# Performance work log

Measured on AMD Instinct MI355X. Metric: run time of the kernel, lower is better.

Reference implementation:

```python
import jax, jax.numpy as jnp
import numpy as np

GROUPS = 16
GROUP_SIZE = 16
K = 3
KK = K * K
BN_EPS = 1e-5


def setup_inputs() -> dict:
    key = jax.random.key(0)
    ks = jax.random.split(key, 6)
    B, C, H, W = 16, 256, 56, 56
    mid = C // 4  # rd_ratio = 4
    x = jax.random.normal(ks[0], (B, C, H, W), dtype=jnp.float32)
    w1 = jax.random.normal(ks[1], (mid, C), dtype=jnp.float32) * (1.0 / np.sqrt(C))
    bn_gamma = jnp.ones((mid,), dtype=jnp.float32)
    bn_beta = jnp.zeros((mid,), dtype=jnp.float32)
    bn_mean = jax.random.normal(ks[2], (mid,), dtype=jnp.float32) * 0.1
    bn_var = jax.random.uniform(ks[3], (mid,), dtype=jnp.float32, minval=0.5, maxval=1.5)
    w2 = jax.random.normal(ks[4], (KK * GROUPS, mid), dtype=jnp.float32) * (1.0 / np.sqrt(mid))
    b2 = jax.random.normal(ks[5], (KK * GROUPS,), dtype=jnp.float32) * 0.01
    return {"x": x, "w1": w1, "bn_gamma": bn_gamma, "bn_beta": bn_beta,
            "bn_mean": bn_mean, "bn_var": bn_var, "w2": w2, "b2": b2}


def reference(x, w1, bn_gamma, bn_beta, bn_mean, bn_var, w2, b2):
    B, C, H, W = x.shape
    # conv1: 1x1 conv + BatchNorm (eval) + ReLU
    t = jnp.einsum('bchw,oc->bohw', x, w1)
    scale = bn_gamma / jnp.sqrt(bn_var + BN_EPS)
    t = t * scale[None, :, None, None] + (bn_beta - bn_mean * scale)[None, :, None, None]
    t = jax.nn.relu(t)
    # conv2: 1x1 conv producing per-pixel kernels (B, KK*groups, H, W)
    weight = jnp.einsum('bchw,oc->bohw', t, w2) + b2[None, :, None, None]
    weight = weight.reshape(B, GROUPS, 1, KK, H, W)
    # unfold: extract 3x3 patches (pad=1, stride=1), kernel positions row-major
    xp = jnp.pad(x, ((0, 0), (0, 0), (1, 1), (1, 1)))
    patches = jnp.stack(
        [xp[:, :, i:i + H, j:j + W] for i in range(K) for j in range(K)],
        axis=2)  # (B, C, KK, H, W), matches torch unfold's (c*KK + kk) layout
    patches = patches.reshape(B, GROUPS, GROUP_SIZE, KK, H, W)
    out = (weight * patches).sum(axis=3).reshape(B, C, H, W)
    return out
```

## Files before the change

kernel.cpp:

```cpp
#include <hip/hip_runtime.h>


#define Cn    256
#define MID   64
#define Hn    56
#define Wn    56
#define HW    3136
#define Bn    16
#define NPIX  (Bn * HW)
#define CHW   (Cn * HW)
#define NKK   9
#define NG    16
#define GSZ   16
#define PXT   64
#define BN_EPS 1e-5f

__global__ __launch_bounds__(256) void prep_kernel(
    const float* __restrict__ w1,
    const float* __restrict__ gamma,
    const float* __restrict__ beta,
    const float* __restrict__ mean,
    const float* __restrict__ var,
    float* __restrict__ w1f,
    float* __restrict__ bias1) {
  int idx = blockIdx.x * 256 + threadIdx.x;
  if (idx < MID * Cn) {
    int c = idx >> 6;
    int o = idx & 63;
    float scale = gamma[o] / sqrtf(var[o] + BN_EPS);
    w1f[idx] = w1[o * Cn + c] * scale;
  } else if (idx < MID * Cn + MID) {
    int o = idx - MID * Cn;
    float scale = gamma[o] / sqrtf(var[o] + BN_EPS);
    bias1[o] = beta[o] - mean[o] * scale;
  }
}

__global__ __launch_bounds__(256) void conv1_kernel(
    const float* __restrict__ x,
    const float* __restrict__ w1f,
    const float* __restrict__ bias1,
    float* __restrict__ t) {
  __shared__ float lx[2][16][PXT];

  int tid = threadIdx.x;
  int px  = tid & 63;
  int ocv = tid >> 6;
  int oc  = __builtin_amdgcn_readfirstlane(ocv);

  int px0 = blockIdx.x * PXT;
  int b   = px0 / HW;
  int hw0 = px0 - b * HW;
  const float* xb = x + (size_t)b * CHW + hw0;

  float r[4];
#pragma unroll
  for (int j = 0; j < 4; ++j) {
    int c = j * 4 + ocv;
    r[j] = xb[(size_t)c * HW + px];
  }
#pragma unroll
  for (int j = 0; j < 4; ++j) lx[0][j * 4 + ocv][px] = r[j];
  __syncthreads();

  float acc[16];
#pragma unroll
  for (int j = 0; j < 16; ++j) acc[j] = 0.0f;

  for (int k = 0; k < 16; ++k) {
    int cur = k & 1;
    if (k < 15) {
#pragma unroll
      for (int j = 0; j < 4; ++j) {
        int c = (k + 1) * 16 + j * 4 + ocv;
        r[j] = xb[(size_t)c * HW + px];
      }
    }
#pragma unroll
    for (int c = 0; c < 16; ++c) {
      float xv = lx[cur][c][px];
      const float* wr = w1f + ((k * 16 + c) << 6) + (oc << 4);
#pragma unroll
      for (int q = 0; q < 4; ++q) {
        float4 w4 = *(const float4*)(wr + q * 4);
        acc[q * 4 + 0] = fmaf(xv, w4.x, acc[q * 4 + 0]);
        acc[q * 4 + 1] = fmaf(xv, w4.y, acc[q * 4 + 1]);
        acc[q * 4 + 2] = fmaf(xv, w4.z, acc[q * 4 + 2]);
        acc[q * 4 + 3] = fmaf(xv, w4.w, acc[q * 4 + 3]);
      }
    }
    if (k < 15) {
#pragma unroll
      for (int j = 0; j < 4; ++j) lx[1 - cur][j * 4 + ocv][px] = r[j];
    }
    __syncthreads();
  }

#pragma unroll
  for (int j = 0; j < 16; ++j) {
    int o = oc * 16 + j;
    float v = acc[j] + bias1[o];
    t[(size_t)o * NPIX + px0 + px] = fmaxf(v, 0.0f);
  }
}

__global__ __launch_bounds__(256) void conv2_inv_kernel(
    const float* __restrict__ x,
    const float* __restrict__ t,
    const float* __restrict__ w2,
    const float* __restrict__ b2,
    float* __restrict__ out) {
  __shared__ float lt[MID][PXT];
  __shared__ float lw[NG * NKK][PXT];

  int tid = threadIdx.x;
  int px  = tid & 63;
  int wvv = tid >> 6;
  int wvu = __builtin_amdgcn_readfirstlane(wvv);

  int px0 = blockIdx.x * PXT;
  int b   = px0 / HW;
  int hw0 = px0 - b * HW;

#pragma unroll
  for (int j = 0; j < 16; ++j) {
    int o = j * 4 + wvv;
    lt[o][px] = t[(size_t)o * NPIX + px0 + px];
  }
  __syncthreads();

  for (int gi = 0; gi < 4; ++gi) {
    int g = wvu + gi * 4;
    float a[NKK];
#pragma unroll
    for (int kk = 0; kk < NKK; ++kk) a[kk] = b2[g * NKK + kk];
#pragma unroll 4
    for (int o = 0; o < MID; ++o) {
      float tv = lt[o][px];
      const float* w2o = w2 + o;
#pragma unroll
      for (int kk = 0; kk < NKK; ++kk)
        a[kk] = fmaf(tv, w2o[(g * NKK + kk) * MID], a[kk]);
    }
#pragma unroll
    for (int kk = 0; kk < NKK; ++kk) lw[g * NKK + kk][px] = a[kk];
  }
  __syncthreads();

  int hw = hw0 + px;
  int h  = hw / Wn;
  int w  = hw - h * Wn;

  int off[NKK];
  unsigned vmask = 0;
#pragma unroll
  for (int kk = 0; kk < NKK; ++kk) {
    int di = kk / 3 - 1;
    int dj = kk % 3 - 1;
    int h2 = h + di;
    int w2v = w + dj;
    bool valid = ((unsigned)h2 < (unsigned)Hn) && ((unsigned)w2v < (unsigned)Wn);
    off[kk] = valid ? (h2 * Wn + w2v) : hw;
    vmask |= (valid ? 1u : 0u) << kk;
  }

  const float* xb = x + (size_t)b * CHW;
  float* ob = out + (size_t)b * CHW + hw;

  for (int gi = 0; gi < 4; ++gi) {
    int g = wvu + gi * 4;
    float wk[NKK];
#pragma unroll
    for (int kk = 0; kk < NKK; ++kk)
      wk[kk] = ((vmask >> kk) & 1u) ? lw[g * NKK + kk][px] : 0.0f;

#pragma unroll 4
    for (int cc = 0; cc < GSZ; ++cc) {
      int c = g * GSZ + cc;
      const float* xc = xb + (size_t)c * HW;
      float a = 0.0f;
#pragma unroll
      for (int kk = 0; kk < NKK; ++kk)
        a = fmaf(wk[kk], xc[off[kk]], a);
      ob[(size_t)c * HW] = a;
    }
  }
}

extern "C" void kernel_launch(void* const* d_in, const int* in_sizes, int n_in,
                              void* d_out, int out_size, void* d_ws, size_t ws_size,
                              hipStream_t stream) {
  const float* x     = (const float*)d_in[0];
  const float* w1    = (const float*)d_in[1];
  const float* gamma = (const float*)d_in[2];
  const float* beta  = (const float*)d_in[3];
  const float* mean  = (const float*)d_in[4];
  const float* var   = (const float*)d_in[5];
  const float* w2    = (const float*)d_in[6];
  const float* b2    = (const float*)d_in[7];
  float* out = (float*)d_out;

  char* ws = (char*)d_ws;
  float* t     = (float*)ws;
  float* w1f   = (float*)(ws + (size_t)MID * NPIX * 4);
  float* bias1 = (float*)(ws + (size_t)MID * NPIX * 4 + (size_t)MID * Cn * 4);

  prep_kernel<<<(MID * Cn + MID + 255) / 256, 256, 0, stream>>>(
      w1, gamma, beta, mean, var, w1f, bias1);
  conv1_kernel<<<NPIX / PXT, 256, 0, stream>>>(x, w1f, bias1, t);
  conv2_inv_kernel<<<NPIX / PXT, 256, 0, stream>>>(x, t, w2, b2, out);
}
```

Before: 192.3 us.

## Fuse conv1, weight generation and involution into one kernel with LDS staging

Merges the conv1 kernel and the conv2/involution kernel into one fused kernel, so the 64-channel intermediate t no longer goes through global memory. x tiles and the folded w1 weights are double-buffered into LDS with global_load_lds direct-to-LDS loads. w2 is staged into a shared LDS buffer, and each wave computes its per-pixel kernel weights in registers right before the involution loop. This removes a large intermediate write and read plus one launch. In exchange it uses more LDS per block, which may lower occupancy, and adds reliance on the async LDS load builtin.

```diff
diff --git a/kernel.cpp b/kernel.cpp
--- a/kernel.cpp
+++ b/kernel.cpp
@@ -14,6 +14,11 @@
 #define GSZ   16
 #define PXT   64
 #define BN_EPS 1e-5f
+
+#define GLOAD_LDS(src, dst, sz)                                                        \
+  __builtin_amdgcn_global_load_lds(                                                    \
+      (const __attribute__((address_space(1))) void*)(src),                            \
+      (__attribute__((address_space(3))) void*)(dst), (sz), 0, 0)
 
 __global__ __launch_bounds__(256) void prep_kernel(
     const float* __restrict__ w1,
@@ -36,153 +41,147 @@
   }
 }
 
-__global__ __launch_bounds__(256) void conv1_kernel(
+__global__ __launch_bounds__(256) void fused_kernel(
     const float* __restrict__ x,
     const float* __restrict__ w1f,
     const float* __restrict__ bias1,
-    float* __restrict__ t) {
-  __shared__ float lx[2][16][PXT];
-
-  int tid = threadIdx.x;
-  int px  = tid & 63;
-  int ocv = tid >> 6;
-  int oc  = __builtin_amdgcn_readfirstlane(ocv);
-
-  int px0 = blockIdx.x * PXT;
-  int b   = px0 / HW;
-  int hw0 = px0 - b * HW;
-  const float* xb = x + (size_t)b * CHW + hw0;
-
-  float r[4];
-#pragma unroll
-  for (int j = 0; j < 4; ++j) {
-    int c = j * 4 + ocv;
-    r[j] = xb[(size_t)c * HW + px];
-  }
-#pragma unroll
-  for (int j = 0; j < 4; ++j) lx[0][j * 4 + ocv][px] = r[j];
-  __syncthreads();
-
-  float acc[16];
-#pragma unroll
-  for (int j = 0; j < 16; ++j) acc[j] = 0.0f;
-
-  for (int k = 0; k < 16; ++k) {
-    int cur = k & 1;
-    if (k < 15) {
-#pragma unroll
-      for (int j = 0; j < 4; ++j) {
-        int c = (k + 1) * 16 + j * 4 + ocv;
-        r[j] = xb[(size_t)c * HW + px];
-      }
-    }
-#pragma unroll
-    for (int c = 0; c < 16; ++c) {
-      float xv = lx[cur][c][px];
-      const float* wr = w1f + ((k * 16 + c) << 6) + (oc << 4);
-#pragma unroll
-      for (int q = 0; q < 4; ++q) {
-        float4 w4 = *(const float4*)(wr + q * 4);
-        acc[q * 4 + 0] = fmaf(xv, w4.x, acc[q * 4 + 0]);
-        acc[q * 4 + 1] = fmaf(xv, w4.y, acc[q * 4 + 1]);
-        acc[q * 4 + 2] = fmaf(xv, w4.z, acc[q * 4 + 2]);
-        acc[q * 4 + 3] = fmaf(xv, w4.w, acc[q * 4 + 3]);
-      }
-    }
-    if (k < 15) {
-#pragma unroll
-      for (int j = 0; j < 4; ++j) lx[1 - cur][j * 4 + ocv][px] = r[j];
-    }
-    __syncthreads();
-  }
-
-#pragma unroll
-  for (int j = 0; j < 16; ++j) {
-    int o = oc * 16 + j;
-    float v = acc[j] + bias1[o];
-    t[(size_t)o * NPIX + px0 + px] = fmaxf(v, 0.0f);
-  }
-}
-
-__global__ __launch_bounds__(256) void conv2_inv_kernel(
-    const float* __restrict__ x,
-    const float* __restrict__ t,
     const float* __restrict__ w2,
     const float* __restrict__ b2,
     float* __restrict__ out) {
   __shared__ float lt[MID][PXT];
-  __shared__ float lw[NG * NKK][PXT];
-
-  int tid = threadIdx.x;
-  int px  = tid & 63;
-  int wvv = tid >> 6;
-  int wvu = __builtin_amdgcn_readfirstlane(wvv);
-
-  int px0 = blockIdx.x * PXT;
-  int b   = px0 / HW;
-  int hw0 = px0 - b * HW;
+  __shared__ __align__(16) float uni[9216];
+
+  const int tid = threadIdx.x;
+  const int px  = tid & 63;
+  const int wvv = tid >> 6;
+  const int wv  = __builtin_amdgcn_readfirstlane(wvv);
+
+  const int px0 = blockIdx.x * PXT;
+  const int b   = px0 / HW;
+  const int hw0 = px0 - b * HW;
+  const float* xb = x + (size_t)b * CHW + hw0;
+
+  {
+#pragma unroll
+    for (int j = 0; j < 4; ++j) {
+      const int c = (wv << 2) + j;
+      GLOAD_LDS(xb + (size_t)c * HW + px, &uni[c * 64], 4);
+    }
+    GLOAD_LDS(w1f + (wv << 8) + (px << 2), &uni[2048 + (wv << 8)], 16);
+  }
+  __syncthreads();
+
+  float acc[16];
+#pragma unroll
+  for (int j = 0; j < 16; ++j) acc[j] = 0.0f;
+
+  for (int k = 0; k < 16; ++k) {
+    const int cur = k & 1;
+    if (k < 15) {
+      const int nb = cur ^ 1;
+      const int kb = k + 1;
+#pragma unroll
+      for (int j = 0; j < 4; ++j) {
+        const int c = (wv << 2) + j;
+        GLOAD_LDS(xb + (size_t)(kb * 16 + c) * HW + px, &uni[nb * 1024 + c * 64], 4);
+      }
+      GLOAD_LDS(w1f + kb * 1024 + (wv << 8) + (px << 2),
+                &uni[2048 + nb * 1024 + (wv << 8)], 16);
+    }
+    const float* lx = &uni[cur * 1024];
+    const float* lw = &uni[2048 + cur * 1024 + (wv << 4)];
+#pragma unroll
+    for (int c = 0; c < 16; ++c) {
+      const float xv = lx[(c << 6) + px];
+      const float4 w40 = *(const float4*)(lw + (c << 6) + 0);
+      const float4 w41 = *(const float4*)(lw + (c << 6) + 4);
+      const float4 w42 = *(const float4*)(lw + (c << 6) + 8);
+      const float4 w43 = *(const float4*)(lw + (c << 6) + 12);
+      acc[0]  = fmaf(xv, w40.x, acc[0]);
+      acc[1]  = fmaf(xv, w40.y, acc[1]);
+      acc[2]  = fmaf(xv, w40.z, acc[2]);
+      acc[3]  = fmaf(xv, w40.w, acc[3]);
+      acc[4]  = fmaf(xv, w41.x, acc[4]);
+      acc[5]  = fmaf(xv, w41.y, acc[5]);
+      acc[6]  = fmaf(xv, w41.z, acc[6]);
+      acc[7]  = fmaf(xv, w41.w, acc[7]);
+      acc[8]  = fmaf(xv, w42.x, acc[8]);
+      acc[9]  = fmaf(xv, w42.y, acc[9]);
+      acc[10] = fmaf(xv, w42.z, acc[10]);
+      acc[11] = fmaf(xv, w42.w, acc[11]);
+      acc[12] = fmaf(xv, w43.x, acc[12]);
+      acc[13] = fmaf(xv, w43.y, acc[13]);
+      acc[14] = fmaf(xv, w43.z, acc[14]);
+      acc[15] = fmaf(xv, w43.w, acc[15]);
+    }
+    __syncthreads();
+  }
 
 #pragma unroll
   for (int j = 0; j < 16; ++j) {
-    int o = j * 4 + wvv;
-    lt[o][px] = t[(size_t)o * NPIX + px0 + px];
+    const int o = (wv << 4) + j;
+    lt[o][px] = fmaxf(acc[j] + bias1[o], 0.0f);
+  }
+#pragma unroll
+  for (int i = 0; i < 9; ++i) {
+    const int r = wv * 9 + i;
+    GLOAD_LDS(w2 + ((size_t)r << 8) + (px << 2), &uni[r << 8], 16);
   }
   __syncthreads();
 
-  for (int gi = 0; gi < 4; ++gi) {
-    int g = wvu + gi * 4;
-    float a[NKK];
-#pragma unroll
-    for (int kk = 0; kk < NKK; ++kk) a[kk] = b2[g * NKK + kk];
-#pragma unroll 4
-    for (int o = 0; o < MID; ++o) {
-      float tv = lt[o][px];
-      const float* w2o = w2 + o;
-#pragma unroll
-      for (int kk = 0; kk < NKK; ++kk)
-        a[kk] = fmaf(tv, w2o[(g * NKK + kk) * MID], a[kk]);
-    }
-#pragma unroll
-    for (int kk = 0; kk < NKK; ++kk) lw[g * NKK + kk][px] = a[kk];
-  }
-  __syncthreads();
-
-  int hw = hw0 + px;
-  int h  = hw / Wn;
-  int w  = hw - h * Wn;
+  const int hw = hw0 + px;
+  const int h  = hw / Wn;
+  const int w  = hw - h * Wn;
 
   int off[NKK];
   unsigned vmask = 0;
 #pragma unroll
   for (int kk = 0; kk < NKK; ++kk) {
-    int di = kk / 3 - 1;
-    int dj = kk % 3 - 1;
-    int h2 = h + di;
-    int w2v = w + dj;
-    bool valid = ((unsigned)h2 < (unsigned)Hn) && ((unsigned)w2v < (unsigned)Wn);
+    const int di  = kk / 3 - 1;
+    const int dj  = kk % 3 - 1;
+    const int h2  = h + di;
+    const int w2v = w + dj;
+    const bool valid = ((unsigned)h2 < (unsigned)Hn) && ((unsigned)w2v < (unsigned)Wn);
     off[kk] = valid ? (h2 * Wn + w2v) : hw;
     vmask |= (valid ? 1u : 0u) << kk;
   }
 
-  const float* xb = x + (size_t)b * CHW;
+  const float* xg = x + (size_t)b * CHW;
   float* ob = out + (size_t)b * CHW + hw;
 
   for (int gi = 0; gi < 4; ++gi) {
-    int g = wvu + gi * 4;
+    const int g = wv + (gi << 2);
+    float a[NKK];
+#pragma unroll
+    for (int kk = 0; kk < NKK; ++kk) a[kk] = b2[g * NKK + kk];
+
+#pragma unroll 4
+    for (int o4 = 0; o4 < MID; o4 += 4) {
+      const float t0 = lt[o4 + 0][px];
+      const float t1 = lt[o4 + 1][px];
+      const float t2 = lt[o4 + 2][px];
+      const float t3 = lt[o4 + 3][px];
+#pragma unroll
+      for (int kk = 0; kk < NKK; ++kk) {
+        const float4 w4 = *(const float4*)&uni[((g * NKK + kk) << 6) + o4];
+        a[kk] = fmaf(t3, w4.w, fmaf(t2, w4.z, fmaf(t1, w4.y, fmaf(t0, w4.x, a[kk]))));
+      }
+    }
+
     float wk[NKK];
 #pragma unroll
     for (int kk = 0; kk < NKK; ++kk)
-      wk[kk] = ((vmask >> kk) & 1u) ? lw[g * NKK + kk][px] : 0.0f;
-
+      wk[kk] = ((vmask >> kk) & 1u) ? a[kk] : 0.0f;
+
+    const float* xc0 = xg + (size_t)(g * GSZ) * HW;
 #pragma unroll 4
     for (int cc = 0; cc < GSZ; ++cc) {
-      int c = g * GSZ + cc;
-      const float* xc = xb + (size_t)c * HW;
-      float a = 0.0f;
+      const float* xc = xc0 + (size_t)cc * HW;
+      float s = 0.0f;
 #pragma unroll
       for (int kk = 0; kk < NKK; ++kk)
-        a = fmaf(wk[kk], xc[off[kk]], a);
-      ob[(size_t)c * HW] = a;
+        s = fmaf(wk[kk], xc[off[kk]], s);
+      ob[(size_t)(g * GSZ + cc) * HW] = s;
     }
   }
 }
@@ -201,12 +200,10 @@
   float* out = (float*)d_out;
 
   char* ws = (char*)d_ws;
-  float* t     = (float*)ws;
-  float* w1f   = (float*)(ws + (size_t)MID * NPIX * 4);
-  float* bias1 = (float*)(ws + (size_t)MID * NPIX * 4 + (size_t)MID * Cn * 4);
+  float* w1f   = (float*)ws;
+  float* bias1 = (float*)(ws + (size_t)MID * Cn * 4);
 
   prep_kernel<<<(MID * Cn + MID + 255) / 256, 256, 0, stream>>>(
       w1, gamma, beta, mean, var, w1f, bias1);
-  conv1_kernel<<<NPIX / PXT, 256, 0, stream>>>(x, w1f, bias1, t);
-  conv2_inv_kernel<<<NPIX / PXT, 256, 0, stream>>>(x, t, w2, b2, out);
+  fused_kernel<<<NPIX / PXT, 256, 0, stream>>>(x, w1f, bias1, w2, b2, out);
 }
```

New measurement: 197.6 us. 2.8% more time.
